# Performance work log

Measured on AMD Instinct MI355X. Metric: run time of the kernel, lower is better.

Reference implementation:

```python
import jax, jax.numpy as jnp
import numpy as np

DECAY = 0.97
TEMP = 0.7
EPS = 1e-6
NORM_EPS = 1e-12  # torch F.normalize default eps


def _l2norm(x, axis=-1):
    n = jnp.linalg.norm(x, axis=axis, keepdims=True)
    return x / jnp.maximum(n, NORM_EPS)


def setup_inputs() -> dict:
    key = jax.random.key(0)
    k1, k2, k3 = jax.random.split(key, 3)
    pair_embed = jax.random.normal(k1, (8, 2048, 1024), dtype=jnp.float32)
    patterns = _l2norm(jax.random.normal(k2, (4096, 1024), dtype=jnp.float32))
    usage = jax.random.uniform(k3, (4096,), dtype=jnp.float32)
    return {"pair_embed": pair_embed, "patterns": patterns, "usage": usage}


def reference(pair_embed, patterns, usage):
    G, D = patterns.shape
    flat = pair_embed.reshape(-1, D)                      # [N, D]
    queries = _l2norm(flat)
    pat_n = _l2norm(patterns)
    logits = queries @ pat_n.T                             # [N, G]
    homeostasis = jnp.log(jnp.clip(usage, EPS))
    weights = jax.nn.softmax((logits - homeostasis[None, :]) / TEMP, axis=-1)

    # Hebbian EMA update (mirrors update(); no_grad in original)
    flat_assign = weights                                  # [N, G]
    weights_sum = flat_assign.sum(axis=0)                  # [G]
    valid = weights_sum > 0
    usage_new = usage * DECAY
    usage_new = jnp.where(valid, usage_new + (1.0 - DECAY) * weights_sum, usage_new)
    updates = flat_assign.T @ flat                         # [G, D]
    updates = updates / (weights_sum[:, None] + EPS)
    blended = _l2norm(patterns * DECAY + (1.0 - DECAY) * updates)
    patterns_new = jnp.where(valid[:, None], blended, patterns)

    out_weights = weights.reshape(*pair_embed.shape[:-1], G)
    return out_weights, patterns_new, usage_new
```

## Files before the change

### kernel.cpp

```cpp
#include <hip/hip_runtime.h>
#include <stdint.h>
#include <math.h>


#define DECAY 0.97f
#define OMD 0.03f
#define INV_TEMP (1.0f / 0.7f)
#define EPS 1e-6f
#define NORM_EPS 1e-12f

constexpr int NROWS = 16384;
constexpr int DK = 1024;
constexpr int GP = 4096;

typedef unsigned short u16;
typedef __bf16 bf16x8 __attribute__((ext_vector_type(8)));
typedef float f32x4 __attribute__((ext_vector_type(4)));

__device__ inline u16 f2bf(float x) {
    union { float f; uint32_t u; } c; c.f = x;
    uint32_t r = c.u + 0x7fffu + ((c.u >> 16) & 1u);
    return (u16)(r >> 16);
}

__device__ inline void gl_lds16(const u16* g, u16* l) {
    __builtin_amdgcn_global_load_lds(
        (const __attribute__((address_space(1))) void*)g,
        (__attribute__((address_space(3))) void*)l, 16, 0, 0);
}

__global__ __launch_bounds__(256) void norm_rows_kernel(
        const float* __restrict__ in, u16* __restrict__ outn) {
    __shared__ float sred[4];
    const int row = blockIdx.x;
    const int t = threadIdx.x;
    const float4 v = ((const float4*)(in + (size_t)row * DK))[t];
    float ss = v.x * v.x + v.y * v.y + v.z * v.z + v.w * v.w;
#pragma unroll
    for (int o = 32; o > 0; o >>= 1) ss += __shfl_xor(ss, o);
    if ((t & 63) == 0) sred[t >> 6] = ss;
    __syncthreads();
    const float tot = sred[0] + sred[1] + sred[2] + sred[3];
    const float rs = 1.0f / fmaxf(sqrtf(tot), NORM_EPS);
    ushort4 o4;
    o4.x = f2bf(v.x * rs); o4.y = f2bf(v.y * rs);
    o4.z = f2bf(v.z * rs); o4.w = f2bf(v.w * rs);
    ((ushort4*)(outn + (size_t)row * DK))[t] = o4;
}

__global__ __launch_bounds__(256) void prep_scalars_kernel(
        const float* __restrict__ usage, float* __restrict__ hscaled,
        float* __restrict__ wsum, float* __restrict__ rowsum) {
    const int i = blockIdx.x * 256 + threadIdx.x;
    if (i < GP) {
        hscaled[i] = logf(fmaxf(usage[i], EPS)) * INV_TEMP;
        wsum[i] = 0.0f;
    }
    rowsum[i] = 0.0f;
}

__global__ __launch_bounds__(256) void rowinv_kernel(float* __restrict__ rowsum) {
    const int i = blockIdx.x * 256 + threadIdx.x;
    rowsum[i] = 1.0f / rowsum[i];
}

__global__ __launch_bounds__(256) void zero_kernel(float4* __restrict__ p) {
    p[(size_t)blockIdx.x * 256 + threadIdx.x] = (float4){0.f, 0.f, 0.f, 0.f};
}

__global__ __launch_bounds__(256) void transpose_f32_bf16_kernel(
        const float* __restrict__ in, u16* __restrict__ out, int R, int C) {
    __shared__ float tile[64][260];
    const int r0 = blockIdx.x * 64;
    const int c0 = blockIdx.y * 256;
    const int t = threadIdx.x;
    const int fr = t & 63;
    const int rr = t >> 6;
#pragma unroll
    for (int j = 0; j < 16; ++j) {
        const int r = rr + 4 * j;
        const float4 v = *(const float4*)(in + (size_t)(r0 + r) * C + c0 + fr * 4);
        *(float4*)&tile[r][fr * 4] = v;
    }
    __syncthreads();
    __align__(16) u16 tmp[64];
#pragma unroll
    for (int r = 0; r < 64; ++r) tmp[r] = f2bf(tile[r][t]);
    u16* op = out + (size_t)(c0 + t) * R + r0;
#pragma unroll
    for (int i = 0; i < 8; ++i) ((uint4*)op)[i] = ((const uint4*)tmp)[i];
}

__global__ __launch_bounds__(256) void scale_transpose_kernel(
        float* __restrict__ W, const float* __restrict__ invs,
        u16* __restrict__ wT, float* __restrict__ wsum) {
    __shared__ float tile[64][260];
    __shared__ float sinv[64];
    const int r0 = blockIdx.x * 64;
    const int c0 = blockIdx.y * 256;
    const int t = threadIdx.x;
    if (t < 64) sinv[t] = invs[r0 + t];
    __syncthreads();
    const int fr = t & 63;
    const int rr = t >> 6;
#pragma unroll
    for (int j = 0; j < 16; ++j) {
        const int r = rr + 4 * j;
        float4 v = *(const float4*)(W + (size_t)(r0 + r) * GP + c0 + fr * 4);
        const float s = sinv[r];
        v.x *= s; v.y *= s; v.z *= s; v.w *= s;
        *(float4*)(W + (size_t)(r0 + r) * GP + c0 + fr * 4) = v;
        *(float4*)&tile[r][fr * 4] = v;
    }
    __syncthreads();
    __align__(16) u16 tmp[64];
    float csum = 0.f;
#pragma unroll
    for (int r = 0; r < 64; ++r) {
        const float x = tile[r][t];
        csum += x;
        tmp[r] = f2bf(x);
    }
    u16* op = wT + (size_t)(c0 + t) * NROWS + r0;
#pragma unroll
    for (int i = 0; i < 8; ++i) ((uint4*)op)[i] = ((const uint4*)tmp)[i];
    atomicAdd(&wsum[c0 + t], csum);
}

template <int KSTEPS, int KLD>
__device__ inline void gemm_bt_256x128(const u16* __restrict__ A,
                                       const u16* __restrict__ B,
                                       int m0, int n0, int k0,
                                       u16* sm, f32x4 acc[4][4]) {
    constexpr int SLOT = 24576;
    constexpr int BOFF = 16384;
    const int t = threadIdx.x;
    const int lane = t & 63;
    const int wave = t >> 6;
    const int wm = (wave >> 1) * 64;
    const int wn = (wave & 1) * 64;
    const int fr = lane & 15;
    const int q8 = lane >> 4;

    const int arow = 32 * wave + (lane >> 3);
    const int brow = 16 * wave + (lane >> 3);
    const size_t a_base = (size_t)(m0 + arow) * KLD + k0 + (((lane & 7) ^ (arow & 7)) * 8);
    const size_t b_base = (size_t)(n0 + brow) * KLD + k0 + (((lane & 7) ^ (brow & 7)) * 8);

    auto STAGE = [&](int slot, int kt) {
        u16* sa = sm + slot * SLOT;
        u16* sb = sa + BOFF;
#pragma unroll
        for (int i = 0; i < 4; ++i)
            gl_lds16(A + a_base + (size_t)(8 * i) * KLD + kt,
                     sa + (32 * wave + 8 * i) * 64);
#pragma unroll
        for (int i = 0; i < 2; ++i)
            gl_lds16(B + b_base + (size_t)(8 * i) * KLD + kt,
                     sb + (16 * wave + 8 * i) * 64);
    };

    STAGE(0, 0);
    STAGE(1, 64);
    asm volatile("s_waitcnt vmcnt(6)" ::: "memory");
    __builtin_amdgcn_sched_barrier(0);
    __builtin_amdgcn_s_barrier();
    __builtin_amdgcn_sched_barrier(0);

    int slot = 0;
#pragma unroll 1
    for (int kt = 0; kt < KSTEPS; kt += 64) {
        if (kt + 128 < KSTEPS) {
            int ss = slot + 2; if (ss >= 3) ss -= 3;
            STAGE(ss, kt + 128);
        }
        const u16* sa = sm + slot * SLOT;
        const u16* sb = sa + BOFF;
#pragma unroll
        for (int ks8 = 0; ks8 < 8; ks8 += 4) {
            bf16x8 af[4], bfr[4];
#pragma unroll
            for (int f = 0; f < 4; ++f) {
                const int ra = wm + f * 16 + fr;
                af[f]  = *(const bf16x8*)(sa + ra * 64 + (((ks8 + q8) ^ (ra & 7)) * 8));
                const int rb = wn + f * 16 + fr;
                bfr[f] = *(const bf16x8*)(sb + rb * 64 + (((ks8 + q8) ^ (rb & 7)) * 8));
            }
            __builtin_amdgcn_s_setprio(1);
#pragma unroll
            for (int fm = 0; fm < 4; ++fm)
#pragma unroll
                for (int fn = 0; fn < 4; ++fn)
                    acc[fm][fn] = __builtin_amdgcn_mfma_f32_16x16x32_bf16(
                        af[fm], bfr[fn], acc[fm][fn], 0, 0, 0);
            __builtin_amdgcn_s_setprio(0);
        }
        if (kt + 128 < KSTEPS) {
            asm volatile("s_waitcnt vmcnt(6)" ::: "memory");
        } else if (kt + 64 < KSTEPS) {
            asm volatile("s_waitcnt vmcnt(0)" ::: "memory");
        }
        __builtin_amdgcn_sched_barrier(0);
        __builtin_amdgcn_s_barrier();
        __builtin_amdgcn_sched_barrier(0);
        slot = slot + 1; if (slot >= 3) slot -= 3;
    }
}

__global__ __launch_bounds__(512) void gemm1_kernel(
        const u16* __restrict__ Q, const u16* __restrict__ P,
        const float* __restrict__ hs, float* __restrict__ Wout,
        float* __restrict__ rowsum) {
    __shared__ u16 sm[3 * 24576];
    const int bid = blockIdx.x;
    const int m0 = (bid >> 5) * 256;
    const int n0 = (bid & 31) * 128;
    f32x4 acc[4][4];
#pragma unroll
    for (int a = 0; a < 4; ++a)
#pragma unroll
        for (int b = 0; b < 4; ++b) acc[a][b] = (f32x4){0.f, 0.f, 0.f, 0.f};
    gemm_bt_256x128<DK, DK>(Q, P, m0, n0, 0, sm, acc);

    const int lane = threadIdx.x & 63;
    const int wave = threadIdx.x >> 6;
    const int wm = (wave >> 1) * 64, wn = (wave & 1) * 64;
    const int cq = lane & 15, rq = (lane >> 4) * 4;
    float hval[4];
#pragma unroll
    for (int fn = 0; fn < 4; ++fn) hval[fn] = hs[n0 + wn + fn * 16 + cq];
#pragma unroll
    for (int fm = 0; fm < 4; ++fm) {
        const int mb = m0 + wm + fm * 16 + rq;
#pragma unroll
        for (int r = 0; r < 4; ++r) {
            float rs = 0.f;
#pragma unroll
            for (int fn = 0; fn < 4; ++fn) {
                const int g = n0 + wn + fn * 16 + cq;
                const float e = __expf(acc[fm][fn][r] * INV_TEMP - hval[fn]);
                Wout[(size_t)(mb + r) * GP + g] = e;
                rs += e;
            }
#pragma unroll
            for (int o = 1; o < 16; o <<= 1) rs += __shfl_xor(rs, o);
            if (cq == 0) atomicAdd(&rowsum[mb + r], rs);
        }
    }
}

__global__ __launch_bounds__(512) void gemm2_kernel(
        const u16* __restrict__ WT, const u16* __restrict__ FT,
        float* __restrict__ Upart) {
    __shared__ u16 sm[3 * 24576];
    const int bid = blockIdx.x;
    const int k0 = (bid & 7) * 2048;
    const int n0 = ((bid >> 3) & 7) * 128;
    const int m0 = (bid >> 6) * 256;
    f32x4 acc[4][4];
#pragma unroll
    for (int a = 0; a < 4; ++a)
#pragma unroll
        for (int b = 0; b < 4; ++b) acc[a][b] = (f32x4){0.f, 0.f, 0.f, 0.f};
    gemm_bt_256x128<2048, NROWS>(WT, FT, m0, n0, k0, sm, acc);

    const int lane = threadIdx.x & 63;
    const int wave = threadIdx.x >> 6;
    const int wm = (wave >> 1) * 64, wn = (wave & 1) * 64;
    const int cq = lane & 15, rq = (lane >> 4) * 4;
#pragma unroll
    for (int fn = 0; fn < 4; ++fn) {
        const int d = n0 + wn + fn * 16 + cq;
#pragma unroll
        for (int fm = 0; fm < 4; ++fm) {
            const int gb = m0 + wm + fm * 16 + rq;
#pragma unroll
            for (int r = 0; r < 4; ++r)
                atomicAdd(&Upart[(size_t)(gb + r) * DK + d], acc[fm][fn][r]);
        }
    }
}

__global__ __launch_bounds__(256) void usage_kernel(
        const float* __restrict__ usage, const float* __restrict__ wsum,
        float* __restrict__ Uout, float* __restrict__ invw) {
    const int g = blockIdx.x * 256 + threadIdx.x;
    if (g < GP) {
        const float s = wsum[g];
        Uout[g] = usage[g] * DECAY + (s > 0.f ? OMD * s : 0.f);
        invw[g] = 1.0f / (s + EPS);
    }
}

__global__ __launch_bounds__(256) void finalize_patterns_kernel(
        const float* __restrict__ patterns, const float* __restrict__ wsum,
        const float* __restrict__ invw, const float* __restrict__ Upart,
        float* __restrict__ Pout) {
    __shared__ float sred[4];
    const int g = blockIdx.x;
    const int t = threadIdx.x;
    const float iw = invw[g] * OMD;
    const float4 u4 = ((const float4*)(Upart + (size_t)g * DK))[t];
    const float4 p4 = ((const float4*)(patterns + (size_t)g * DK))[t];
    float4 b;
    b.x = DECAY * p4.x + iw * u4.x;
    b.y = DECAY * p4.y + iw * u4.y;
    b.z = DECAY * p4.z + iw * u4.z;
    b.w = DECAY * p4.w + iw * u4.w;
    float ss = b.x * b.x + b.y * b.y + b.z * b.z + b.w * b.w;
#pragma unroll
    for (int o = 32; o > 0; o >>= 1) ss += __shfl_xor(ss, o);
    if ((t & 63) == 0) sred[t >> 6] = ss;
    __syncthreads();
    const float tot = sred[0] + sred[1] + sred[2] + sred[3];
    const float rs = 1.0f / fmaxf(sqrtf(tot), NORM_EPS);
    float4 o4;
    if (wsum[g] > 0.f) {
        o4.x = b.x * rs; o4.y = b.y * rs; o4.z = b.z * rs; o4.w = b.w * rs;
    } else {
        o4 = p4;
    }
    ((float4*)(Pout + (size_t)g * DK))[t] = o4;
}

extern "C" void kernel_launch(void* const* d_in, const int* in_sizes, int n_in,
                              void* d_out, int out_size, void* d_ws, size_t ws_size,
                              hipStream_t stream) {
    const float* pair_embed = (const float*)d_in[0];
    const float* patterns   = (const float*)d_in[1];
    const float* usage      = (const float*)d_in[2];

    float* out_w = (float*)d_out;
    float* out_p = out_w + (size_t)NROWS * GP;
    float* out_u = out_p + (size_t)GP * DK;

    char* ws = (char*)d_ws;
    u16* q_bf   = (u16*)(ws);
    float* Upart = (float*)(ws);
    u16* pat_bf = (u16*)(ws + 33554432);
    u16* fT     = (u16*)(ws + 41943040);
    u16* wT     = (u16*)(ws + 75497472);
    float* hs   = (float*)(ws + 209715200);
    float* wsum = (float*)(ws + 209715200 + 16384);
    float* invw = (float*)(ws + 209715200 + 32768);
    float* rsum = (float*)(ws + 209715200 + 49152);

    prep_scalars_kernel<<<64, 256, 0, stream>>>(usage, hs, wsum, rsum);
    norm_rows_kernel<<<NROWS, 256, 0, stream>>>(pair_embed, q_bf);
    norm_rows_kernel<<<GP, 256, 0, stream>>>(patterns, pat_bf);
    {
        dim3 g(NROWS / 64, DK / 256);
        transpose_f32_bf16_kernel<<<g, 256, 0, stream>>>(pair_embed, fT, NROWS, DK);
    }
    gemm1_kernel<<<(NROWS / 256) * (GP / 128), 512, 0, stream>>>(q_bf, pat_bf, hs, out_w, rsum);
    rowinv_kernel<<<64, 256, 0, stream>>>(rsum);
    {
        dim3 g(NROWS / 64, GP / 256);
        scale_transpose_kernel<<<g, 256, 0, stream>>>(out_w, rsum, wT, wsum);
    }
    usage_kernel<<<16, 256, 0, stream>>>(usage, wsum, out_u, invw);
    zero_kernel<<<(GP * DK / 4) / 256, 256, 0, stream>>>((float4*)Upart);
    gemm2_kernel<<<8 * (GP / 256) * (DK / 128), 512, 0, stream>>>(wT, fT, Upart);
    finalize_patterns_kernel<<<GP, 256, 0, stream>>>(patterns, wsum, invw, Upart, out_p);
}
```

Baseline: 894.5 us.

## Enlarge GEMM tiles to 256x256 with double-buffered LDS and fewer split-K partitions

Both GEMMs move from 256x128 to 256x256 block tiles, with each wave computing a 128x64 sub-tile (8x4 MFMA fragments). The LDS pipeline drops from triple to double buffering, and gemm2 uses 4 split-K partitions instead of 8. The larger tiles raise arithmetic intensity per LDS and global load and halve the number of atomic adds in gemm2. In exchange, accumulator register pressure doubles, fewer blocks are launched (1024 for gemm1, 256 for gemm2), and the shallower prefetch gives less latency hiding.

After: 826.6 us. 7.6% less time.

```diff
diff --git a/kernel.cpp b/kernel.cpp
--- a/kernel.cpp
+++ b/kernel.cpp
@@ -128,41 +128,39 @@
 }
 
 template <int KSTEPS, int KLD>
-__device__ inline void gemm_bt_256x128(const u16* __restrict__ A,
+__device__ inline void gemm_bt_256x256(const u16* __restrict__ A,
                                        const u16* __restrict__ B,
                                        int m0, int n0, int k0,
-                                       u16* sm, f32x4 acc[4][4]) {
-    constexpr int SLOT = 24576;
+                                       u16* sm, f32x4 acc[8][4]) {
+    constexpr int SLOT = 32768;
     constexpr int BOFF = 16384;
     const int t = threadIdx.x;
     const int lane = t & 63;
     const int wave = t >> 6;
-    const int wm = (wave >> 1) * 64;
-    const int wn = (wave & 1) * 64;
+    const int wm = (wave >> 2) * 128;
+    const int wn = (wave & 3) * 64;
     const int fr = lane & 15;
     const int q8 = lane >> 4;
 
-    const int arow = 32 * wave + (lane >> 3);
-    const int brow = 16 * wave + (lane >> 3);
-    const size_t a_base = (size_t)(m0 + arow) * KLD + k0 + (((lane & 7) ^ (arow & 7)) * 8);
-    const size_t b_base = (size_t)(n0 + brow) * KLD + k0 + (((lane & 7) ^ (brow & 7)) * 8);
+    const int srow = 32 * wave + (lane >> 3);
+    const int soct = (lane & 7) ^ (srow & 7);
+    const size_t a_base = (size_t)(m0 + srow) * KLD + k0 + soct * 8;
+    const size_t b_base = (size_t)(n0 + srow) * KLD + k0 + soct * 8;
 
     auto STAGE = [&](int slot, int kt) {
         u16* sa = sm + slot * SLOT;
         u16* sb = sa + BOFF;
 #pragma unroll
-        for (int i = 0; i < 4; ++i)
+        for (int i = 0; i < 4; ++i) {
             gl_lds16(A + a_base + (size_t)(8 * i) * KLD + kt,
                      sa + (32 * wave + 8 * i) * 64);
-#pragma unroll
-        for (int i = 0; i < 2; ++i)
             gl_lds16(B + b_base + (size_t)(8 * i) * KLD + kt,
-                     sb + (16 * wave + 8 * i) * 64);
+                     sb + (32 * wave + 8 * i) * 64);
+        }
     };
 
     STAGE(0, 0);
-    STAGE(1, 64);
-    asm volatile("s_waitcnt vmcnt(6)" ::: "memory");
+    asm volatile("s_waitcnt vmcnt(0)" ::: "memory");
     __builtin_amdgcn_sched_barrier(0);
     __builtin_amdgcn_s_barrier();
     __builtin_amdgcn_sched_barrier(0);
@@ -170,67 +168,65 @@
     int slot = 0;
 #pragma unroll 1
     for (int kt = 0; kt < KSTEPS; kt += 64) {
-        if (kt + 128 < KSTEPS) {
-            int ss = slot + 2; if (ss >= 3) ss -= 3;
-            STAGE(ss, kt + 128);
-        }
+        if (kt + 64 < KSTEPS) STAGE(slot ^ 1, kt + 64);
         const u16* sa = sm + slot * SLOT;
         const u16* sb = sa + BOFF;
 #pragma unroll
         for (int ks8 = 0; ks8 < 8; ks8 += 4) {
-            bf16x8 af[4], bfr[4];
-#pragma unroll
-            for (int f = 0; f < 4; ++f) {
+            bf16x8 af[8], bfr[4];
+#pragma unroll
+            for (int f = 0; f < 8; ++f) {
                 const int ra = wm + f * 16 + fr;
                 af[f]  = *(const bf16x8*)(sa + ra * 64 + (((ks8 + q8) ^ (ra & 7)) * 8));
+            }
+#pragma unroll
+            for (int f = 0; f < 4; ++f) {
                 const int rb = wn + f * 16 + fr;
                 bfr[f] = *(const bf16x8*)(sb + rb * 64 + (((ks8 + q8) ^ (rb & 7)) * 8));
             }
             __builtin_amdgcn_s_setprio(1);
 #pragma unroll
-            for (int fm = 0; fm < 4; ++fm)
+            for (int fm = 0; fm < 8; ++fm)
 #pragma unroll
                 for (int fn = 0; fn < 4; ++fn)
                     acc[fm][fn] = __builtin_amdgcn_mfma_f32_16x16x32_bf16(
                         af[fm], bfr[fn], acc[fm][fn], 0, 0, 0);
             __builtin_amdgcn_s_setprio(0);
         }
-        if (kt + 128 < KSTEPS) {
-            asm volatile("s_waitcnt vmcnt(6)" ::: "memory");
-        } else if (kt + 64 < KSTEPS) {
+        if (kt + 64 < KSTEPS) {
             asm volatile("s_waitcnt vmcnt(0)" ::: "memory");
-        }
-        __builtin_amdgcn_sched_barrier(0);
-        __builtin_amdgcn_s_barrier();
-        __builtin_amdgcn_sched_barrier(0);
-        slot = slot + 1; if (slot >= 3) slot -= 3;
-    }
-}
-
-__global__ __launch_bounds__(512) void gemm1_kernel(
+            __builtin_amdgcn_sched_barrier(0);
+            __builtin_amdgcn_s_barrier();
+            __builtin_amdgcn_sched_barrier(0);
+        }
+        slot ^= 1;
+    }
+}
+
+__global__ __launch_bounds__(512, 2) void gemm1_kernel(
         const u16* __restrict__ Q, const u16* __restrict__ P,
         const float* __restrict__ hs, float* __restrict__ Wout,
         float* __restrict__ rowsum) {
-    __shared__ u16 sm[3 * 24576];
+    __shared__ u16 sm[2 * 32768];
     const int bid = blockIdx.x;
-    const int m0 = (bid >> 5) * 256;
-    const int n0 = (bid & 31) * 128;
-    f32x4 acc[4][4];
-#pragma unroll
-    for (int a = 0; a < 4; ++a)
+    const int m0 = (bid >> 4) * 256;
+    const int n0 = (bid & 15) * 256;
+    f32x4 acc[8][4];
+#pragma unroll
+    for (int a = 0; a < 8; ++a)
 #pragma unroll
         for (int b = 0; b < 4; ++b) acc[a][b] = (f32x4){0.f, 0.f, 0.f, 0.f};
-    gemm_bt_256x128<DK, DK>(Q, P, m0, n0, 0, sm, acc);
+    gemm_bt_256x256<DK, DK>(Q, P, m0, n0, 0, sm, acc);
 
     const int lane = threadIdx.x & 63;
     const int wave = threadIdx.x >> 6;
-    const int wm = (wave >> 1) * 64, wn = (wave & 1) * 64;
+    const int wm = (wave >> 2) * 128, wn = (wave & 3) * 64;
     const int cq = lane & 15, rq = (lane >> 4) * 4;
     float hval[4];
 #pragma unroll
     for (int fn = 0; fn < 4; ++fn) hval[fn] = hs[n0 + wn + fn * 16 + cq];
 #pragma unroll
-    for (int fm = 0; fm < 4; ++fm) {
+    for (int fm = 0; fm < 8; ++fm) {
         const int mb = m0 + wm + fm * 16 + rq;
 #pragma unroll
         for (int r = 0; r < 4; ++r) {
@@ -249,30 +245,30 @@
     }
 }
 
-__global__ __launch_bounds__(512) void gemm2_kernel(
+__global__ __launch_bounds__(512, 2) void gemm2_kernel(
         const u16* __restrict__ WT, const u16* __restrict__ FT,
         float* __restrict__ Upart) {
-    __shared__ u16 sm[3 * 24576];
+    __shared__ u16 sm[2 * 32768];
     const int bid = blockIdx.x;
-    const int k0 = (bid & 7) * 2048;
-    const int n0 = ((bid >> 3) & 7) * 128;
-    const int m0 = (bid >> 6) * 256;
-    f32x4 acc[4][4];
-#pragma unroll
-    for (int a = 0; a < 4; ++a)
+    const int k0 = (bid & 3) * 4096;
+    const int n0 = ((bid >> 2) & 3) * 256;
+    const int m0 = (bid >> 4) * 256;
+    f32x4 acc[8][4];
+#pragma unroll
+    for (int a = 0; a < 8; ++a)
 #pragma unroll
         for (int b = 0; b < 4; ++b) acc[a][b] = (f32x4){0.f, 0.f, 0.f, 0.f};
-    gemm_bt_256x128<2048, NROWS>(WT, FT, m0, n0, k0, sm, acc);
+    gemm_bt_256x256<4096, NROWS>(WT, FT, m0, n0, k0, sm, acc);
 
     const int lane = threadIdx.x & 63;
     const int wave = threadIdx.x >> 6;
-    const int wm = (wave >> 1) * 64, wn = (wave & 1) * 64;
+    const int wm = (wave >> 2) * 128, wn = (wave & 3) * 64;
     const int cq = lane & 15, rq = (lane >> 4) * 4;
 #pragma unroll
     for (int fn = 0; fn < 4; ++fn) {
         const int d = n0 + wn + fn * 16 + cq;
 #pragma unroll
-        for (int fm = 0; fm < 4; ++fm) {
+        for (int fm = 0; fm < 8; ++fm) {
             const int gb = m0 + wm + fm * 16 + rq;
 #pragma unroll
             for (int r = 0; r < 4; ++r)
@@ -352,7 +348,7 @@
         dim3 g(NROWS / 64, DK / 256);
         transpose_f32_bf16_kernel<<<g, 256, 0, stream>>>(pair_embed, fT, NROWS, DK);
     }
-    gemm1_kernel<<<(NROWS / 256) * (GP / 128), 512, 0, stream>>>(q_bf, pat_bf, hs, out_w, rsum);
+    gemm1_kernel<<<(NROWS / 256) * (GP / 256), 512, 0, stream>>>(q_bf, pat_bf, hs, out_w, rsum);
     rowinv_kernel<<<64, 256, 0, stream>>>(rsum);
     {
         dim3 g(NROWS / 64, GP / 256);
@@ -360,6 +356,6 @@
     }
     usage_kernel<<<16, 256, 0, stream>>>(usage, wsum, out_u, invw);
     zero_kernel<<<(GP * DK / 4) / 256, 256, 0, stream>>>((float4*)Upart);
-    gemm2_kernel<<<8 * (GP / 256) * (DK / 128), 512, 0, stream>>>(wT, fT, Upart);
+    gemm2_kernel<<<4 * (GP / 256) * (DK / 256), 512, 0, stream>>>(wT, fT, Upart);
     finalize_patterns_kernel<<<GP, 256, 0, stream>>>(patterns, wsum, invw, Upart, out_p);
 }
```
